# Kernel optimization log

Hardware: AMD Instinct MI355X
Metric: run time of the kernel (lower is better)

Reference implementation:

```python
import jax, jax.numpy as jnp
import numpy as np

B, S, D, H = 2, 2048, 1024, 16
DEPTH = D // H


def setup_inputs() -> dict:
    key = jax.random.key(0)
    ks = jax.random.split(key, 10)
    batch = jax.random.normal(ks[0], (B, S, D), dtype=jnp.float32)
    # variable-length valid rows, like padded batches in the original repo
    lengths = jax.random.randint(ks[1], (B,), S // 2, S + 1)
    mask = jnp.arange(S)[None, :] < lengths[:, None]  # (B, S) bool
    scale = 1.0 / np.sqrt(D)
    Wq = jax.random.normal(ks[2], (D, D), dtype=jnp.float32) * scale
    bq = jnp.zeros((D,), dtype=jnp.float32)
    Wk = jax.random.normal(ks[3], (D, D), dtype=jnp.float32) * scale
    bk = jnp.zeros((D,), dtype=jnp.float32)
    Wv = jax.random.normal(ks[4], (D, D), dtype=jnp.float32) * scale
    bv = jnp.zeros((D,), dtype=jnp.float32)
    Wo = jax.random.normal(ks[5], (D, D), dtype=jnp.float32) * scale
    bo = jnp.zeros((D,), dtype=jnp.float32)
    return {"batch": batch, "mask": mask, "Wq": Wq, "bq": bq, "Wk": Wk,
            "bk": bk, "Wv": Wv, "bv": bv, "Wo": Wo, "bo": bo}


def _split_heads(x):
    # (B, S, D) -> (B, H, S, depth)
    b, s, _ = x.shape
    return x.reshape(b, s, H, DEPTH).transpose(0, 2, 1, 3)


def reference(batch, mask, Wq, bq, Wk, bk, Wv, bv, Wo, bo):
    b, s, _ = batch.shape
    Q = _split_heads(batch @ Wq + bq)
    K = _split_heads(batch @ Wk + bk)
    V = _split_heads(batch @ Wv + bv)
    # scaled dot-product attention with key-padding mask
    logits = jnp.einsum('bhqd,bhkd->bhqk', Q, K) / jnp.sqrt(
        jnp.asarray(DEPTH, dtype=batch.dtype))
    neg = (~mask).astype(batch.dtype) * -1e9  # (B, S)
    logits = logits + neg[:, None, None, :]
    attn = jax.nn.softmax(logits, axis=-1)
    X = jnp.einsum('bhqk,bhkd->bhqd', attn, V)
    X = X.transpose(0, 2, 1, 3).reshape(b, s, D)
    return X @ Wo + bo
```

## Files before the change

### kernel.cpp

```cpp
#include <hip/hip_runtime.h>
#include <hip/hip_bf16.h>

#define DEV __device__ __forceinline__

typedef short bf16x8 __attribute__((ext_vector_type(8)));
typedef float f32x4  __attribute__((ext_vector_type(4)));

#define Bc 2
#define Sc 2048
#define Dc 1024
#define Hc 16

#define OFF_XB    0u
#define OFF_WQKVT 8388608u
#define OFF_WOT   14680064u
#define OFF_Q     16777216u
#define OFF_K     25165824u
#define OFF_VT    33554432u
#define OFF_XA    41943040u
#define OFF_BIASC 50331648u
#define OFF_LENS  50343936u

DEV short f2bf(float f) {
    __hip_bfloat16 h = __float2bfloat16(f);
    union { __hip_bfloat16 h; short s; } u; u.h = h; return u.s;
}

DEV int cvtpk(float lo, float hi_) {
    int r;
    asm("v_cvt_pk_bf16_f32 %0, %1, %2" : "=v"(r) : "v"(lo), "v"(hi_));
    return r;
}

DEV float vexp2(float x) {
    float r;
    asm("v_exp_f32 %0, %1" : "=v"(r) : "v"(x));
    return r;
}

DEV void gload16(const void* g, void* l) {
    __builtin_amdgcn_global_load_lds((const __attribute__((address_space(1))) void*)g,
                                     (__attribute__((address_space(3))) void*)l, 16, 0, 0);
}

union I4BF { int i[4]; bf16x8 v; };

__global__ __launch_bounds__(256) void prep_all_kernel(
    const float* __restrict__ batch,
    const float* __restrict__ Wq, const float* __restrict__ Wk,
    const float* __restrict__ Wv, const float* __restrict__ Wo,
    const float* __restrict__ bq, const float* __restrict__ bk, const float* __restrict__ bv,
    const unsigned char* __restrict__ mask,
    short* __restrict__ XB, short* __restrict__ WQKVT, short* __restrict__ WOT,
    float* __restrict__ biasc, int* __restrict__ lens)
{
    __shared__ float tsm[32][33];
    __shared__ int cnt;
    int blk = blockIdx.x, t = threadIdx.x;

    if (blk < 4096) {
        int i = blk * 256 + t;
        float4 v = ((const float4*)batch)[i];
        short4 o;
        o.x = f2bf(v.x); o.y = f2bf(v.y); o.z = f2bf(v.z); o.w = f2bf(v.w);
        ((short4*)XB)[i] = o;
        return;
    }
    if (blk < 8192) {
        int w = blk - 4096, z = w >> 10, tile = w & 1023;
        const float* src; short* dst;
        if (z == 0)      { src = Wq; dst = WQKVT; }
        else if (z == 1) { src = Wk; dst = WQKVT + 1024 * 1024; }
        else if (z == 2) { src = Wv; dst = WQKVT + 2 * 1024 * 1024; }
        else             { src = Wo; dst = WOT; }
        int tx = t & 31, ty = t >> 5;
        int r0 = (tile >> 5) * 32, c0 = (tile & 31) * 32;
#pragma unroll
        for (int i = 0; i < 4; i++)
            tsm[ty + i * 8][tx] = src[(size_t)(r0 + ty + i * 8) * Dc + c0 + tx];
        __syncthreads();
#pragma unroll
        for (int i = 0; i < 4; i++)
            dst[(size_t)(c0 + ty + i * 8) * Dc + r0 + tx] = f2bf(tsm[tx][ty + i * 8]);
        return;
    }
    if (blk == 8192) {
        for (int i = t; i < Dc; i += 256) {
            biasc[i] = bq[i]; biasc[Dc + i] = bk[i]; biasc[2 * Dc + i] = bv[i];
        }
        return;
    }
    {
        int b = blk - 8193;
        bool is_i32 = (mask[1] == 0);
        if (t == 0) cnt = 0;
        __syncthreads();
        int local = 0;
        for (int s = t; s < Sc; s += 256) {
            bool v = is_i32 ? (((const int*)mask)[b * Sc + s] != 0) : (mask[b * Sc + s] != 0);
            local += v ? 1 : 0;
        }
        atomicAdd(&cnt, local);
        __syncthreads();
        if (t == 0) lens[b] = cnt;
    }
}

__global__ __launch_bounds__(256) void vtrans_kernel(const short* __restrict__ V,
                                                     short* __restrict__ VT,
                                                     const int* __restrict__ lens) {
    __shared__ short t[64][65];
    int tid = threadIdx.x;
    int bh = blockIdx.y, s0 = blockIdx.x * 64;
    int b = bh >> 4;
    int kv_end = ((lens[b] + 63) >> 6) << 6;
    if (s0 >= kv_end) return;
    int rr = tid >> 2, c4 = (tid & 3) * 16;
    const short* vrow = V + ((size_t)bh * Sc + s0 + rr) * 64 + c4;
    *(bf16x8*)&t[rr][c4]     = *(const bf16x8*)(vrow);
    *(bf16x8*)&t[rr][c4 + 8] = *(const bf16x8*)(vrow + 8);
    __syncthreads();
    int q2 = tid & 3;
    int gidx = q2 >> 1, half = q2 & 1;
    int base = gidx * 32, off = half * 8;
    bf16x8 a, b2;
#pragma unroll
    for (int i = 0; i < 4; i++) {
        a[i]      = t[base + off + i][rr];
        a[4 + i]  = t[base + 16 + off + i][rr];
        b2[i]     = t[base + off + 4 + i][rr];
        b2[4 + i] = t[base + 16 + off + 4 + i][rr];
    }
    short* orow = VT + ((size_t)bh * 64 + rr) * Sc + s0 + base + half * 16;
    *(bf16x8*)(orow)     = a;
    *(bf16x8*)(orow + 8) = b2;
}

__global__ __launch_bounds__(256) void gemm_qkv_kernel(
    const short* __restrict__ A, const short* __restrict__ BT, const float* __restrict__ bias,
    short* __restrict__ Qp, short* __restrict__ Kp, short* __restrict__ Vp,
    const int* __restrict__ lens)
{
    __shared__ short As[128 * 32];
    __shared__ short Bs[128 * 32];
    int tid = threadIdx.x, lane = tid & 63, wave = tid >> 6;
    int l15 = lane & 15, lhi = lane >> 4;
    int bm = blockIdx.x, bn = blockIdx.y;

    if (bn >= 8) {
        int brow = bm >> 4;
        int s_lo = (bm & 15) * 128;
        int kv_end = ((lens[brow] + 63) >> 6) << 6;
        if (s_lo >= kv_end) return;
    }

    int wm = wave >> 1, wn = wave & 1;

    const f32x4 fzero = {0.f, 0.f, 0.f, 0.f};
    f32x4 acc[4][4];
#pragma unroll
    for (int i = 0; i < 4; i++)
#pragma unroll
        for (int j = 0; j < 4; j++) acc[i][j] = fzero;

    const char* Ab = (const char*)A;
    const char* Bb = (const char*)BT;

    for (int k0 = 0; k0 < 1024; k0 += 32) {
#pragma unroll
        for (int i = 0; i < 2; i++) {
            int o = wave * 2048 + i * 1024 + lane * 16;
            int row = o >> 6, cb = o & 63;
            gload16(Ab + ((size_t)(bm * 128 + row) * 1024 + k0) * 2 + cb,
                    (char*)As + wave * 2048 + i * 1024);
            gload16(Bb + ((size_t)(bn * 128 + row) * 1024 + k0) * 2 + cb,
                    (char*)Bs + wave * 2048 + i * 1024);
        }
        __syncthreads();
        bf16x8 af[4], bfv[4];
#pragma unroll
        for (int i = 0; i < 4; i++) {
            af[i]  = *(const bf16x8*)(As + (wm * 64 + i * 16 + l15) * 32 + lhi * 8);
            bfv[i] = *(const bf16x8*)(Bs + (wn * 64 + i * 16 + l15) * 32 + lhi * 8);
        }
#pragma unroll
        for (int i = 0; i < 4; i++)
#pragma unroll
            for (int j = 0; j < 4; j++)
                acc[i][j] = __builtin_amdgcn_mfma_f32_16x16x32_bf16(af[i], bfv[j], acc[i][j], 0, 0, 0);
        __syncthreads();
    }

#pragma unroll
    for (int i = 0; i < 4; i++)
#pragma unroll
        for (int j = 0; j < 4; j++) {
            int c = bn * 128 + wn * 64 + j * 16 + l15;
            float bc = bias[c];
            int rb = bm * 128 + wm * 64 + i * 16 + 4 * lhi;
#pragma unroll
            for (int reg = 0; reg < 4; reg++) {
                int r = rb + reg;
                float v = acc[i][j][reg] + bc;
                int which = c >> 10, cc = c & 1023, h = cc >> 6, d = cc & 63;
                int b = r >> 11, s = r & 2047;
                int bh = b * Hc + h;
                if (which == 0) v *= 0.18033688f;
                short sv = f2bf(v);
                size_t idx = ((size_t)bh * Sc + s) * 64 + d;
                if (which == 0)      Qp[idx] = sv;
                else if (which == 1) Kp[idx] = sv;
                else                 Vp[idx] = sv;
            }
        }
}

__global__ __launch_bounds__(256) void gemm_out_kernel(
    const short* __restrict__ A, const short* __restrict__ BT, const float* __restrict__ bias,
    float* __restrict__ outF)
{
    __shared__ short As[128 * 32];
    __shared__ short Bs[64 * 32];
    int tid = threadIdx.x, lane = tid & 63, wave = tid >> 6;
    int l15 = lane & 15, lhi = lane >> 4;
    int bm = blockIdx.x, bn = blockIdx.y;

    const f32x4 fzero = {0.f, 0.f, 0.f, 0.f};
    f32x4 acc[2][4];
#pragma unroll
    for (int i = 0; i < 2; i++)
#pragma unroll
        for (int j = 0; j < 4; j++) acc[i][j] = fzero;

    const char* Ab = (const char*)A;
    const char* Bb = (const char*)BT;

    for (int k0 = 0; k0 < 1024; k0 += 32) {
#pragma unroll
        for (int i = 0; i < 2; i++) {
            int o = wave * 2048 + i * 1024 + lane * 16;
            int row = o >> 6, cb = o & 63;
            gload16(Ab + ((size_t)(bm * 128 + row) * 1024 + k0) * 2 + cb,
                    (char*)As + wave * 2048 + i * 1024);
        }
        {
            int o = wave * 1024 + lane * 16;
            int row = o >> 6, cb = o & 63;
            gload16(Bb + ((size_t)(bn * 64 + row) * 1024 + k0) * 2 + cb,
                    (char*)Bs + wave * 1024);
        }
        __syncthreads();
        bf16x8 af[2], bfv[4];
#pragma unroll
        for (int i = 0; i < 2; i++)
            af[i] = *(const bf16x8*)(As + (wave * 32 + i * 16 + l15) * 32 + lhi * 8);
#pragma unroll
        for (int j = 0; j < 4; j++)
            bfv[j] = *(const bf16x8*)(Bs + (j * 16 + l15) * 32 + lhi * 8);
#pragma unroll
        for (int i = 0; i < 2; i++)
#pragma unroll
            for (int j = 0; j < 4; j++)
                acc[i][j] = __builtin_amdgcn_mfma_f32_16x16x32_bf16(af[i], bfv[j], acc[i][j], 0, 0, 0);
        __syncthreads();
    }

#pragma unroll
    for (int i = 0; i < 2; i++)
#pragma unroll
        for (int j = 0; j < 4; j++) {
            int c = bn * 64 + j * 16 + l15;
            float bc = bias[c];
            int rb = bm * 128 + wave * 32 + i * 16 + 4 * lhi;
#pragma unroll
            for (int reg = 0; reg < 4; reg++)
                outF[(size_t)(rb + reg) * Dc + c] = acc[i][j][reg] + bc;
        }
}

__global__ __launch_bounds__(256) void attn_kernel(
    const short* __restrict__ Qp, const short* __restrict__ Kp, const short* __restrict__ VTp,
    const int* __restrict__ lens, short* __restrict__ Xout)
{
    int tid = threadIdx.x, lane = tid & 63, wave = tid >> 6;
    int l15 = lane & 15, g4 = lane >> 4;

    int orig = blockIdx.x;
    int xcd = orig & 7, idx = orig >> 3;
    int j = idx & 3, bx = idx >> 2;
    int bh = ((j >> 1) << 4) + xcd * 2 + (j & 1);
    int b = bh >> 4, h = bh & 15;
    int q0 = bx * 64 + wave * 16;

    __shared__ short Kt[2][64 * 64];
    __shared__ short Vt[2][64 * 64];

    const short* Qb  = Qp + (size_t)bh * Sc * 64;
    const char*  Kb  = (const char*)(Kp + (size_t)bh * Sc * 64);
    const char*  VTb = (const char*)(VTp + (size_t)bh * 64 * Sc);

    bf16x8 qf0 = *(const bf16x8*)(Qb + (size_t)(q0 + l15) * 64 + g4 * 8);
    bf16x8 qf1 = *(const bf16x8*)(Qb + (size_t)(q0 + l15) * 64 + 32 + g4 * 8);

    const f32x4 FZ = {0.f, 0.f, 0.f, 0.f};
    f32x4 xacc[4];
#pragma unroll
    for (int dt = 0; dt < 4; dt++) xacc[dt] = FZ;
    float lreg = 0.f;

    int len = lens[b];
    int nt = (len + 63) >> 6;
    int rsw = (l15 & 7) << 4;
    int g16 = g4 * 16;

#define STAGE(bufi, kt_)                                                              \
    {                                                                                 \
        int k0_ = (kt_) * 64;                                                         \
        _Pragma("unroll")                                                             \
        for (int i = 0; i < 2; i++) {                                                 \
            int o = i * 4096 + tid * 16;                                              \
            int row = o >> 7, cb = o & 127;                                           \
            int scb = cb ^ ((row & 7) << 4);                                          \
            gload16(Kb + (size_t)(k0_ + row) * 128 + scb,                             \
                    (char*)&Kt[bufi][0] + o);                                         \
            gload16(VTb + (size_t)row * (Sc * 2) + (size_t)k0_ * 2 + scb,             \
                    (char*)&Vt[bufi][0] + o);                                         \
        }                                                                             \
    }

#define DOTILE(BUFI, KT)                                                              \
    {                                                                                 \
        const char* Kc = (const char*)&Kt[BUFI][0];                                   \
        const char* Vc = (const char*)&Vt[BUFI][0];                                   \
        f32x4 s[4];                                                                   \
        __builtin_amdgcn_s_setprio(1);                                                \
        _Pragma("unroll")                                                             \
        for (int k16 = 0; k16 < 4; k16++) {                                           \
            const char* kr = Kc + (k16 * 16 + l15) * 128;                             \
            bf16x8 kf0 = *(const bf16x8*)(kr + (g16 ^ rsw));                          \
            bf16x8 kf1 = *(const bf16x8*)(kr + ((64 + g16) ^ rsw));                   \
            s[k16] = __builtin_amdgcn_mfma_f32_16x16x32_bf16(kf0, qf0, FZ, 0, 0, 0);  \
            s[k16] = __builtin_amdgcn_mfma_f32_16x16x32_bf16(kf1, qf1, s[k16], 0, 0, 0);\
        }                                                                             \
        __builtin_amdgcn_s_setprio(0);                                                \
        if ((KT) == nt - 1) {                                                         \
            int rem = len - (KT) * 64;                                                \
            if (rem < 64) {                                                           \
                _Pragma("unroll")                                                     \
                for (int k16 = 0; k16 < 4; k16++)                                     \
                    _Pragma("unroll")                                                 \
                    for (int r = 0; r < 4; r++) {                                     \
                        int key0 = k16 * 16 + 4 * g4 + r;                             \
                        if (key0 >= rem) s[k16][r] = -3.0e38f;                        \
                    }                                                                 \
            }                                                                         \
        }                                                                             \
        _Pragma("unroll")                                                             \
        for (int k16 = 0; k16 < 4; k16++)                                             \
            _Pragma("unroll")                                                         \
            for (int r = 0; r < 4; r++) s[k16][r] = vexp2(s[k16][r]);                 \
        {                                                  \
            float a0 = (s[0][0] + s[0][1]) + (s[0][2] + s[0][3]);                     \
            float a1 = (s[1][0] + s[1][1]) + (s[1][2] + s[1][3]);                     \
            float a2 = (s[2][0] + s[2][1]) + (s[2][2] + s[2][3]);                     \
            float a3 = (s[3][0] + s[3][1]) + (s[3][2] + s[3][3]);                     \
            lreg += (a0 + a1) + (a2 + a3);                                            \
        }                                                                             \
           \
        I4BF p0, p1;                                                                  \
        p0.i[0] = cvtpk(s[0][0], s[0][1]); p0.i[1] = cvtpk(s[0][2], s[0][3]);         \
        p0.i[2] = cvtpk(s[1][0], s[1][1]); p0.i[3] = cvtpk(s[1][2], s[1][3]);         \
        p1.i[0] = cvtpk(s[2][0], s[2][1]); p1.i[1] = cvtpk(s[2][2], s[2][3]);         \
        p1.i[2] = cvtpk(s[3][0], s[3][1]); p1.i[3] = cvtpk(s[3][2], s[3][3]);         \
        __builtin_amdgcn_s_setprio(1);                                                \
        _Pragma("unroll")                                                             \
        for (int dt = 0; dt < 4; dt++) {                                              \
            const char* vr = Vc + (dt * 16 + l15) * 128;                              \
            bf16x8 v0 = *(const bf16x8*)(vr + (g16 ^ rsw));                           \
            bf16x8 v1 = *(const bf16x8*)(vr + ((64 + g16) ^ rsw));                    \
            xacc[dt] = __builtin_amdgcn_mfma_f32_16x16x32_bf16(v0, p0.v, xacc[dt], 0, 0, 0);\
            xacc[dt] = __builtin_amdgcn_mfma_f32_16x16x32_bf16(v1, p1.v, xacc[dt], 0, 0, 0);\
        }                                                                             \
        __builtin_amdgcn_s_setprio(0);                                                \
    }

    STAGE(0, 0);
    __syncthreads();

    int kt = 0;
    while (kt + 2 <= nt) {
        if (kt + 1 < nt) STAGE(1, kt + 1);
        DOTILE(0, kt);
        __syncthreads();
        if (kt + 2 < nt) STAGE(0, kt + 2);
        DOTILE(1, kt + 1);
        __syncthreads();
        kt += 2;
    }
    if (kt < nt) DOTILE(0, kt);

    float lfull = lreg + __shfl_xor(lreg, 16, 64);
    lfull += __shfl_xor(lfull, 32, 64);
    float rl = 1.0f / lfull;
    short* orow = Xout + (size_t)(b * Sc + q0 + l15) * Dc + h * 64;
#pragma unroll
    for (int dt = 0; dt < 4; dt++) {
        short4 o;
        o.x = f2bf(xacc[dt][0] * rl);
        o.y = f2bf(xacc[dt][1] * rl);
        o.z = f2bf(xacc[dt][2] * rl);
        o.w = f2bf(xacc[dt][3] * rl);
        *(short4*)(orow + dt * 16 + 4 * g4) = o;
    }
}


extern "C" void kernel_launch(void* const* d_in, const int* in_sizes, int n_in,
                              void* d_out, int out_size, void* d_ws, size_t ws_size,
                              hipStream_t stream) {
    const float* batch = (const float*)d_in[0];
    const unsigned char* mask = (const unsigned char*)d_in[1];
    const float* Wq = (const float*)d_in[2];
    const float* bq = (const float*)d_in[3];
    const float* Wk = (const float*)d_in[4];
    const float* bk = (const float*)d_in[5];
    const float* Wv = (const float*)d_in[6];
    const float* bv = (const float*)d_in[7];
    const float* Wo = (const float*)d_in[8];
    const float* bo = (const float*)d_in[9];

    char* ws = (char*)d_ws;
    short* XB    = (short*)(ws + OFF_XB);
    short* WQKVT = (short*)(ws + OFF_WQKVT);
    short* WOT   = (short*)(ws + OFF_WOT);
    short* Qb    = (short*)(ws + OFF_Q);
    short* Kb    = (short*)(ws + OFF_K);
    short* VTb   = (short*)(ws + OFF_VT);
    short* XAb   = (short*)(ws + OFF_XA);
    float* BIASC = (float*)(ws + OFF_BIASC);
    int*   LENS  = (int*)(ws + OFF_LENS);
    short* Vscr  = (short*)d_out;

    prep_all_kernel<<<8195, 256, 0, stream>>>(batch, Wq, Wk, Wv, Wo, bq, bk, bv, mask,
                                              XB, WQKVT, WOT, BIASC, LENS);
    gemm_qkv_kernel<<<dim3(32, 24), 256, 0, stream>>>(XB, WQKVT, BIASC, Qb, Kb, Vscr, LENS);
    vtrans_kernel<<<dim3(32, 32), 256, 0, stream>>>(Vscr, VTb, LENS);
    attn_kernel<<<1024, 256, 0, stream>>>(Qb, Kb, VTb, LENS, XAb);
    gemm_out_kernel<<<dim3(32, 16), 256, 0, stream>>>(XAb, WOT, bo, (float*)d_out);
}
```

Measured before the change: 119.3 us.

## Double GEMM K-step with XOR-swizzled LDS; compute softmax row sums via MFMA

Both projection GEMMs now stage 64-wide K slices per iteration into XOR-swizzled shared memory. This halves the number of barriers per output tile and spreads LDS bank accesses to reduce conflicts, at the cost of doubling LDS per block. In the attention kernel, the per-lane VALU summation of exponentials and the final cross-lane shuffles are replaced by an extra MFMA against a vector of ones. The bf16-rounded probabilities then form the softmax denominator, which also makes normalisation consistent with the P·V product.

```diff
diff --git a/kernel.cpp b/kernel.cpp
--- a/kernel.cpp
+++ b/kernel.cpp
@@ -141,8 +141,8 @@
     short* __restrict__ Qp, short* __restrict__ Kp, short* __restrict__ Vp,
     const int* __restrict__ lens)
 {
-    __shared__ short As[128 * 32];
-    __shared__ short Bs[128 * 32];
+    __shared__ short As[128 * 64];
+    __shared__ short Bs[128 * 64];
     int tid = threadIdx.x, lane = tid & 63, wave = tid >> 6;
     int l15 = lane & 15, lhi = lane >> 4;
     int bm = blockIdx.x, bn = blockIdx.y;
@@ -155,6 +155,7 @@
     }
 
     int wm = wave >> 1, wn = wave & 1;
+    int rsw = (l15 & 7) << 4;
 
     const f32x4 fzero = {0.f, 0.f, 0.f, 0.f};
     f32x4 acc[4][4];
@@ -166,28 +167,34 @@
     const char* Ab = (const char*)A;
     const char* Bb = (const char*)BT;
 
-    for (int k0 = 0; k0 < 1024; k0 += 32) {
-#pragma unroll
-        for (int i = 0; i < 2; i++) {
-            int o = wave * 2048 + i * 1024 + lane * 16;
-            int row = o >> 6, cb = o & 63;
-            gload16(Ab + ((size_t)(bm * 128 + row) * 1024 + k0) * 2 + cb,
-                    (char*)As + wave * 2048 + i * 1024);
-            gload16(Bb + ((size_t)(bn * 128 + row) * 1024 + k0) * 2 + cb,
-                    (char*)Bs + wave * 2048 + i * 1024);
-        }
-        __syncthreads();
-        bf16x8 af[4], bfv[4];
+    for (int k0 = 0; k0 < 1024; k0 += 64) {
 #pragma unroll
         for (int i = 0; i < 4; i++) {
-            af[i]  = *(const bf16x8*)(As + (wm * 64 + i * 16 + l15) * 32 + lhi * 8);
-            bfv[i] = *(const bf16x8*)(Bs + (wn * 64 + i * 16 + l15) * 32 + lhi * 8);
-        }
-#pragma unroll
-        for (int i = 0; i < 4; i++)
-#pragma unroll
-            for (int j = 0; j < 4; j++)
-                acc[i][j] = __builtin_amdgcn_mfma_f32_16x16x32_bf16(af[i], bfv[j], acc[i][j], 0, 0, 0);
+            int o = i * 4096 + tid * 16;
+            int row = o >> 7, cb = o & 127;
+            int scb = cb ^ ((row & 7) << 4);
+            gload16(Ab + ((size_t)(bm * 128 + row) * 1024 + k0) * 2 + scb, (char*)As + o);
+            gload16(Bb + ((size_t)(bn * 128 + row) * 1024 + k0) * 2 + scb, (char*)Bs + o);
+        }
+        __syncthreads();
+#pragma unroll
+        for (int kk = 0; kk < 2; kk++) {
+            bf16x8 af[4], bfv[4];
+#pragma unroll
+            for (int i = 0; i < 4; i++) {
+                int rowa = wm * 64 + i * 16 + l15;
+                int rowb = wn * 64 + i * 16 + l15;
+                af[i]  = *(const bf16x8*)((char*)As + rowa * 128 +
+                                          ((kk * 64 + lhi * 16) ^ rsw));
+                bfv[i] = *(const bf16x8*)((char*)Bs + rowb * 128 +
+                                          ((kk * 64 + lhi * 16) ^ rsw));
+            }
+#pragma unroll
+            for (int i = 0; i < 4; i++)
+#pragma unroll
+                for (int j = 0; j < 4; j++)
+                    acc[i][j] = __builtin_amdgcn_mfma_f32_16x16x32_bf16(af[i], bfv[j], acc[i][j], 0, 0, 0);
+        }
         __syncthreads();
     }
 
@@ -219,11 +226,12 @@
     const short* __restrict__ A, const short* __restrict__ BT, const float* __restrict__ bias,
     float* __restrict__ outF)
 {
-    __shared__ short As[128 * 32];
-    __shared__ short Bs[64 * 32];
+    __shared__ short As[128 * 64];
+    __shared__ short Bs[64 * 64];
     int tid = threadIdx.x, lane = tid & 63, wave = tid >> 6;
     int l15 = lane & 15, lhi = lane >> 4;
     int bm = blockIdx.x, bn = blockIdx.y;
+    int rsw = (l15 & 7) << 4;
 
     const f32x4 fzero = {0.f, 0.f, 0.f, 0.f};
     f32x4 acc[2][4];
@@ -235,33 +243,43 @@
     const char* Ab = (const char*)A;
     const char* Bb = (const char*)BT;
 
-    for (int k0 = 0; k0 < 1024; k0 += 32) {
+    for (int k0 = 0; k0 < 1024; k0 += 64) {
+#pragma unroll
+        for (int i = 0; i < 4; i++) {
+            int o = i * 4096 + tid * 16;
+            int row = o >> 7, cb = o & 127;
+            int scb = cb ^ ((row & 7) << 4);
+            gload16(Ab + ((size_t)(bm * 128 + row) * 1024 + k0) * 2 + scb, (char*)As + o);
+        }
 #pragma unroll
         for (int i = 0; i < 2; i++) {
-            int o = wave * 2048 + i * 1024 + lane * 16;
-            int row = o >> 6, cb = o & 63;
-            gload16(Ab + ((size_t)(bm * 128 + row) * 1024 + k0) * 2 + cb,
-                    (char*)As + wave * 2048 + i * 1024);
-        }
-        {
-            int o = wave * 1024 + lane * 16;
-            int row = o >> 6, cb = o & 63;
-            gload16(Bb + ((size_t)(bn * 64 + row) * 1024 + k0) * 2 + cb,
-                    (char*)Bs + wave * 1024);
-        }
-        __syncthreads();
-        bf16x8 af[2], bfv[4];
-#pragma unroll
-        for (int i = 0; i < 2; i++)
-            af[i] = *(const bf16x8*)(As + (wave * 32 + i * 16 + l15) * 32 + lhi * 8);
-#pragma unroll
-        for (int j = 0; j < 4; j++)
-            bfv[j] = *(const bf16x8*)(Bs + (j * 16 + l15) * 32 + lhi * 8);
-#pragma unroll
-        for (int i = 0; i < 2; i++)
-#pragma unroll
-            for (int j = 0; j < 4; j++)
-                acc[i][j] = __builtin_amdgcn_mfma_f32_16x16x32_bf16(af[i], bfv[j], acc[i][j], 0, 0, 0);
+            int o = i * 4096 + tid * 16;
+            int row = o >> 7, cb = o & 127;
+            int scb = cb ^ ((row & 7) << 4);
+            gload16(Bb + ((size_t)(bn * 64 + row) * 1024 + k0) * 2 + scb, (char*)Bs + o);
+        }
+        __syncthreads();
+#pragma unroll
+        for (int kk = 0; kk < 2; kk++) {
+            bf16x8 af[2], bfv[4];
+#pragma unroll
+            for (int i = 0; i < 2; i++) {
+                int rowa = wave * 32 + i * 16 + l15;
+                af[i] = *(const bf16x8*)((char*)As + rowa * 128 +
+                                         ((kk * 64 + lhi * 16) ^ rsw));
+            }
+#pragma unroll
+            for (int j = 0; j < 4; j++) {
+                int rowb = j * 16 + l15;
+                bfv[j] = *(const bf16x8*)((char*)Bs + rowb * 128 +
+                                          ((kk * 64 + lhi * 16) ^ rsw));
+            }
+#pragma unroll
+            for (int i = 0; i < 2; i++)
+#pragma unroll
+                for (int j = 0; j < 4; j++)
+                    acc[i][j] = __builtin_amdgcn_mfma_f32_16x16x32_bf16(af[i], bfv[j], acc[i][j], 0, 0, 0);
+        }
         __syncthreads();
     }
 
@@ -302,11 +320,14 @@
     bf16x8 qf0 = *(const bf16x8*)(Qb + (size_t)(q0 + l15) * 64 + g4 * 8);
     bf16x8 qf1 = *(const bf16x8*)(Qb + (size_t)(q0 + l15) * 64 + 32 + g4 * 8);
 
+    bf16x8 onesv;
+#pragma unroll
+    for (int i = 0; i < 8; i++) onesv[i] = (short)0x3F80;
+
     const f32x4 FZ = {0.f, 0.f, 0.f, 0.f};
-    f32x4 xacc[4];
+    f32x4 xacc[4], lacc = FZ;
 #pragma unroll
     for (int dt = 0; dt < 4; dt++) xacc[dt] = FZ;
-    float lreg = 0.f;
 
     int len = lens[b];
     int nt = (len + 63) >> 6;
@@ -359,20 +380,14 @@
         for (int k16 = 0; k16 < 4; k16++)                                             \
             _Pragma("unroll")                                                         \
             for (int r = 0; r < 4; r++) s[k16][r] = vexp2(s[k16][r]);                 \
-        {                                                  \
-            float a0 = (s[0][0] + s[0][1]) + (s[0][2] + s[0][3]);                     \
-            float a1 = (s[1][0] + s[1][1]) + (s[1][2] + s[1][3]);                     \
-            float a2 = (s[2][0] + s[2][1]) + (s[2][2] + s[2][3]);                     \
-            float a3 = (s[3][0] + s[3][1]) + (s[3][2] + s[3][3]);                     \
-            lreg += (a0 + a1) + (a2 + a3);                                            \
-        }                                                                             \
-           \
         I4BF p0, p1;                                                                  \
         p0.i[0] = cvtpk(s[0][0], s[0][1]); p0.i[1] = cvtpk(s[0][2], s[0][3]);         \
         p0.i[2] = cvtpk(s[1][0], s[1][1]); p0.i[3] = cvtpk(s[1][2], s[1][3]);         \
         p1.i[0] = cvtpk(s[2][0], s[2][1]); p1.i[1] = cvtpk(s[2][2], s[2][3]);         \
         p1.i[2] = cvtpk(s[3][0], s[3][1]); p1.i[3] = cvtpk(s[3][2], s[3][3]);         \
         __builtin_amdgcn_s_setprio(1);                                                \
+        lacc = __builtin_amdgcn_mfma_f32_16x16x32_bf16(onesv, p0.v, lacc, 0, 0, 0);   \
+        lacc = __builtin_amdgcn_mfma_f32_16x16x32_bf16(onesv, p1.v, lacc, 0, 0, 0);   \
         _Pragma("unroll")                                                             \
         for (int dt = 0; dt < 4; dt++) {                                              \
             const char* vr = Vc + (dt * 16 + l15) * 128;                              \
@@ -399,9 +414,7 @@
     }
     if (kt < nt) DOTILE(0, kt);
 
-    float lfull = lreg + __shfl_xor(lreg, 16, 64);
-    lfull += __shfl_xor(lfull, 32, 64);
-    float rl = 1.0f / lfull;
+    float rl = 1.0f / lacc[0];
     short* orow = Xout + (size_t)(b * Sc + q0 + l15) * Dc + h * 64;
 #pragma unroll
     for (int dt = 0; dt < 4; dt++) {
```

New measurement: 123.3 us. 1.03x slower.
